# Kernel optimization log

Measured on AMD Instinct MI355X. Metric: run time of the kernel, lower is better.

## Reference

```python
import jax, jax.numpy as jnp
import numpy as np

T = 4096
MOL = 2048
DESC = 6
NSOL = 5
H = 2048
D_BLOCK = MOL + DESC            # 2054
FUSE = D_BLOCK * (1 + NSOL)     # 12324
D_IN = FUSE + 1                 # 12325
BOUNDARY_RF = 0.5
CLAMP_LO, CLAMP_HI = 1e-4, 1.0 - 1e-4


def setup_inputs() -> dict:
    key = jax.random.key(0)
    ks = jax.random.split(key, 32)
    s = 0.02  # weight init scale for numerical stability
    d = {
        "mol_vec": jax.random.normal(ks[0], (MOL,), jnp.float32),
        "solvent_seq": jax.random.uniform(ks[1], (T, NSOL), jnp.float32),
        "desc_seq": jax.random.normal(ks[2], (T, DESC), jnp.float32),
        "rf_true": jax.random.uniform(ks[3], (T,), jnp.float32),
        "solvent_vecs": jax.random.normal(ks[4], (NSOL, MOL), jnp.float32),
    }
    wshapes = [
        ("Wf0", (H, D_IN)), ("Wf1", (H, H)), ("Wf2", (H, H)), ("Wof", (1, H)),
        ("Wb0", (H, D_IN)), ("Wb1", (H, H)), ("Wb2", (H, H)), ("Wob", (1, H)),
    ]
    for i, (name, shp) in enumerate(wshapes):
        d[name] = jax.random.normal(ks[5 + i], shp, jnp.float32) * s
    for name, shp in [("bf0", (H,)), ("bf1", (H,)), ("bf2", (H,)), ("bof", (1,)),
                      ("bb0", (H,)), ("bb1", (H,)), ("bb2", (H,)), ("bob", (1,))]:
        d[name] = jnp.zeros(shp, jnp.float32)
    return d


def _step_features(mol_vec, solvent_seq, desc_seq, solvent_vecs):
    # mol_vec [MOL]; solvent_seq [T,NSOL]; desc_seq [T,DESC]; solvent_vecs [NSOL,MOL]
    mol_cat = jnp.concatenate(
        [jnp.broadcast_to(mol_vec, (T, MOL)), desc_seq], axis=-1)  # [T, D_BLOCK]
    scaled = solvent_seq[:, :, None] * solvent_vecs[None, :, :]      # [T,NSOL,MOL]
    sol_block = jnp.concatenate(
        [scaled, jnp.broadcast_to(desc_seq[:, None, :], (T, NSOL, DESC))], axis=-1)
    sol_flat = sol_block.reshape(T, NSOL * D_BLOCK)
    return jnp.concatenate([mol_cat, sol_flat], axis=-1)             # [T, FUSE]


def _trunk(x, W0, b0, W1, b1, W2, b2):
    # 3 Linear+GELU blocks (dropout is identity in eval)
    h = jax.nn.gelu(x @ W0.T + b0, approximate=False)
    h = jax.nn.gelu(h @ W1.T + b1, approximate=False)
    h = jax.nn.gelu(h @ W2.T + b2, approximate=False)
    return h


def reference(mol_vec, solvent_seq, desc_seq, rf_true, solvent_vecs,
              Wf0, bf0, Wf1, bf1, Wf2, bf2, Wof, bof,
              Wb0, bb0, Wb1, bb1, Wb2, bb2, Wob, bob):
    x = _step_features(mol_vec, solvent_seq, desc_seq, solvent_vecs)  # [T, FUSE]
    rf = jax.lax.stop_gradient(rf_true)  # teacher signal is detached
    b = jnp.asarray([BOUNDARY_RF], dtype=x.dtype)
    prev = jnp.concatenate([b, rf[:-1]])  # fwd branch sees rf_true[t-1]
    nxt = jnp.concatenate([rf[1:], b])    # bwd branch sees rf_true[t+1]

    inp_f = jnp.concatenate([x, prev[:, None]], axis=-1)  # [T, D_IN]
    inp_b = jnp.concatenate([x, nxt[:, None]], axis=-1)

    hf = _trunk(inp_f, Wf0, bf0, Wf1, bf1, Wf2, bf2)
    hb = _trunk(inp_b, Wb0, bb0, Wb1, bb1, Wb2, bb2)
    rf_fwd = (hf @ Wof.T + bof).squeeze(-1)  # [T]
    rf_bwd = (hb @ Wob.T + bob).squeeze(-1)
    rf_fwd = jnp.clip(rf_fwd, CLAMP_LO, CLAMP_HI)
    rf_bwd = jnp.clip(rf_bwd, CLAMP_LO, CLAMP_HI)
    return rf_fwd, rf_bwd
```

## Files before the change

kernel.cpp:

```cpp
#include <hip/hip_runtime.h>
#include <hip/hip_fp16.h>
#include <math.h>

#define T_DIM 4096
#define MOL_N 2048
#define DESC_N 6
#define NSOL_N 5
#define H_DIM 2048
#define DBLK 2054
#define D_IN_N 12325

typedef _Float16 f16x8 __attribute__((ext_vector_type(8)));
typedef float f32x4 __attribute__((ext_vector_type(4)));

__device__ __forceinline__ float gelu_f(float x) {
    float v = x * (1.5957691f + 0.0713548f * x * x);
    float e = __expf(-v);
    return x / (1.0f + e);
}

__global__ __launch_bounds__(256) void fold_kernel(
    const float* __restrict__ W0f, const float* __restrict__ W0b,
    const float* __restrict__ b0f, const float* __restrict__ b0b,
    const float* __restrict__ mol, const float* __restrict__ sv,
    float* __restrict__ fold_f, float* __restrict__ fold_b)
{
    const int h = blockIdx.x;
    const int z = blockIdx.y;
    const float* __restrict__ W0 = z ? W0b : W0f;
    const float* __restrict__ b0 = z ? b0b : b0f;
    float* __restrict__ fold = z ? fold_b : fold_f;
    const float* __restrict__ row = W0 + (size_t)h * D_IN_N;
    const int tid = threadIdx.x;

    float acc[6] = {0.f, 0.f, 0.f, 0.f, 0.f, 0.f};
    #pragma unroll
    for (int i = 0; i < 8; ++i) {
        const int c = tid + i * 256;
        const float m = mol[c];
        acc[0] += row[c] * m;
        #pragma unroll
        for (int s = 0; s < NSOL_N; ++s)
            acc[1 + s] += row[DBLK * (s + 1) + c] * sv[s * MOL_N + c];
    }
    #pragma unroll
    for (int i = 0; i < 6; ++i) {
        float v = acc[i];
        #pragma unroll
        for (int off = 32; off >= 1; off >>= 1)
            v += __shfl_xor(v, off, 64);
        acc[i] = v;
    }
    __shared__ float red[4][6];
    const int lane = tid & 63, wave = tid >> 6;
    if (lane == 0) {
        #pragma unroll
        for (int i = 0; i < 6; ++i) red[wave][i] = acc[i];
    }
    __syncthreads();
    if (tid < 6) {
        float s = red[0][tid] + red[1][tid] + red[2][tid] + red[3][tid];
        if (tid == 0) fold[h] = s + b0[h];
        else fold[(size_t)tid * H_DIM + h] = s;
    }
    if (tid >= 64 && tid < 70) {
        int j = tid - 64;
        float w = row[MOL_N + j];
        #pragma unroll
        for (int s = 0; s < NSOL_N; ++s) w += row[DBLK * (s + 1) + MOL_N + j];
        fold[(size_t)(6 + j) * H_DIM + h] = w;
    }
    if (tid == 70) fold[(size_t)12 * H_DIM + h] = row[D_IN_N - 1];
}

__global__ __launch_bounds__(256) void conv_kernel(
    const float* __restrict__ W1f, const float* __restrict__ W2f,
    const float* __restrict__ W1b, const float* __restrict__ W2b,
    _Float16* __restrict__ dstbase)
{
    const int z = blockIdx.y;
    const float* __restrict__ src = (z == 0) ? W1f : (z == 1) ? W2f : (z == 2) ? W1b : W2b;
    _Float16* __restrict__ dst = dstbase + (size_t)z * H_DIM * H_DIM;
    const int idx = blockIdx.x * 256 + threadIdx.x;
    float4 v = ((const float4*)src)[idx];
    struct h4 { _Float16 a, b, c, d; };
    h4 o;
    o.a = (_Float16)v.x; o.b = (_Float16)v.y; o.c = (_Float16)v.z; o.d = (_Float16)v.w;
    ((h4*)dst)[idx] = o;
}

__global__ __launch_bounds__(256) void h0_kernel(
    const float* __restrict__ fold_f, const float* __restrict__ fold_b,
    const float* __restrict__ desc, const float* __restrict__ sol,
    const float* __restrict__ rf,
    _Float16* __restrict__ h0f, _Float16* __restrict__ h0b)
{
    const int z = blockIdx.z;
    const float* __restrict__ fold = z ? fold_b : fold_f;
    _Float16* __restrict__ h0 = z ? h0b : h0f;
    const int h = blockIdx.x * 256 + threadIdx.x;
    const int tbase = blockIdx.y * 64;

    const float c0 = fold[h];
    float u[NSOL_N], wd[DESC_N];
    #pragma unroll
    for (int s = 0; s < NSOL_N; ++s) u[s] = fold[(size_t)(1 + s) * H_DIM + h];
    #pragma unroll
    for (int j = 0; j < DESC_N; ++j) wd[j] = fold[(size_t)(6 + j) * H_DIM + h];
    const float wp = fold[(size_t)12 * H_DIM + h];

    for (int i = 0; i < 64; ++i) {
        const int t = tbase + i;
        float pv;
        if (z == 0) pv = (t == 0) ? 0.5f : rf[t - 1];
        else        pv = (t == T_DIM - 1) ? 0.5f : rf[t + 1];
        float pre = c0 + wp * pv;
        #pragma unroll
        for (int s = 0; s < NSOL_N; ++s) pre += u[s] * sol[t * NSOL_N + s];
        #pragma unroll
        for (int j = 0; j < DESC_N; ++j) pre += wd[j] * desc[t * DESC_N + j];
        h0[(size_t)t * H_DIM + h] = (_Float16)gelu_f(pre);
    }
}

__global__ __launch_bounds__(256) void gemm_kernel(
    const _Float16* __restrict__ Af, const _Float16* __restrict__ Ab,
    const _Float16* __restrict__ Wfp, const _Float16* __restrict__ Wbp,
    const float* __restrict__ bfp, const float* __restrict__ bbp,
    _Float16* __restrict__ Cf, _Float16* __restrict__ Cb)
{
    constexpr int K = H_DIM;
    constexpr int N = H_DIM;
    const int bid = blockIdx.x;
    const int xcd = bid & 7;
    const int slot = bid >> 3;
    const int z = xcd & 1;
    const int q = xcd >> 1;
    const int m0 = (q * 8 + (slot & 7)) * 128;
    const int n0 = (slot >> 3) * 128;

    const _Float16* __restrict__ A = z ? Ab : Af;
    const _Float16* __restrict__ W = z ? Wbp : Wfp;
    const float* __restrict__ bias = z ? bbp : bfp;
    _Float16* __restrict__ C = z ? Cb : Cf;

    __shared__ _Float16 sA[128 * 64];
    __shared__ _Float16 sB[128 * 64];

    const int tid = threadIdx.x;
    const int wave = tid >> 6;
    const int lane = tid & 63;
    const int quad = lane >> 4;

    char* sAc = (char*)sA;
    char* sBc = (char*)sB;

    const _Float16* gA[4];
    const _Float16* gB[4];
    #pragma unroll
    for (int ld = 0; ld < 4; ++ld) {
        const int j = ld * 256 + tid;
        const int r = j >> 3;
        const int c = (j & 7) ^ (r & 7);
        gA[ld] = A + (size_t)(m0 + r) * K + c * 8;
        gB[ld] = W + (size_t)(n0 + r) * K + c * 8;
    }

    f32x4 acc[4][4];
    #pragma unroll
    for (int i = 0; i < 4; ++i)
        #pragma unroll
        for (int j = 0; j < 4; ++j)
            acc[i][j] = (f32x4){0.f, 0.f, 0.f, 0.f};

    const int rA = (wave & 1) * 64 + (lane & 15);
    const int rB = (wave >> 1) * 64 + (lane & 15);
    const int xorL = lane & 7;

    for (int k0 = 0; k0 < K; k0 += 64) {
        #pragma unroll
        for (int ld = 0; ld < 4; ++ld)
            __builtin_amdgcn_global_load_lds(
                (const __attribute__((address_space(1))) void*)(gA[ld] + k0),
                (__attribute__((address_space(3))) void*)(sAc + ld * 4096 + wave * 1024), 16, 0, 0);
        #pragma unroll
        for (int ld = 0; ld < 4; ++ld)
            __builtin_amdgcn_global_load_lds(
                (const __attribute__((address_space(1))) void*)(gB[ld] + k0),
                (__attribute__((address_space(3))) void*)(sBc + ld * 4096 + wave * 1024), 16, 0, 0);
        __syncthreads();
        #pragma unroll
        for (int kk = 0; kk < 2; ++kk) {
            const int coff = ((kk * 4 + quad) ^ xorL) * 16;
            f16x8 aF[4], bF[4];
            #pragma unroll
            for (int mi = 0; mi < 4; ++mi)
                aF[mi] = *(const f16x8*)(sAc + (rA + mi * 16) * 128 + coff);
            #pragma unroll
            for (int ni = 0; ni < 4; ++ni)
                bF[ni] = *(const f16x8*)(sBc + (rB + ni * 16) * 128 + coff);
            #pragma unroll
            for (int mi = 0; mi < 4; ++mi)
                #pragma unroll
                for (int ni = 0; ni < 4; ++ni)
                    acc[mi][ni] = __builtin_amdgcn_mfma_f32_16x16x32_f16(aF[mi], bF[ni], acc[mi][ni], 0, 0, 0);
        }
        __syncthreads();
    }

    const int colC = lane & 15;
    #pragma unroll
    for (int ni = 0; ni < 4; ++ni) {
        const int n = n0 + (wave >> 1) * 64 + ni * 16 + colC;
        const float bv = bias[n];
        #pragma unroll
        for (int mi = 0; mi < 4; ++mi) {
            const int mb = m0 + (wave & 1) * 64 + mi * 16 + quad * 4;
            #pragma unroll
            for (int r = 0; r < 4; ++r) {
                float v = acc[mi][ni][r] + bv;
                C[(size_t)(mb + r) * N + n] = (_Float16)gelu_f(v);
            }
        }
    }
}

__global__ __launch_bounds__(256) void gemm_out_kernel(
    const _Float16* __restrict__ Af, const _Float16* __restrict__ Ab,
    const _Float16* __restrict__ Wfp, const _Float16* __restrict__ Wbp,
    const float* __restrict__ bfp, const float* __restrict__ bbp,
    const float* __restrict__ Wof, const float* __restrict__ Wob,
    float* __restrict__ out_acc)
{
    constexpr int K = H_DIM;
    const int bid = blockIdx.x;
    const int xcd = bid & 7;
    const int slot = bid >> 3;
    const int z = xcd & 1;
    const int q = xcd >> 1;
    const int m0 = (q * 8 + (slot & 7)) * 128;
    const int n0 = (slot >> 3) * 128;

    const _Float16* __restrict__ A = z ? Ab : Af;
    const _Float16* __restrict__ W = z ? Wbp : Wfp;
    const float* __restrict__ bias = z ? bbp : bfp;
    const float* __restrict__ Wo = z ? Wob : Wof;

    __shared__ _Float16 sA[128 * 64];
    __shared__ _Float16 sB[128 * 64];

    const int tid = threadIdx.x;
    const int wave = tid >> 6;
    const int lane = tid & 63;
    const int quad = lane >> 4;

    char* sAc = (char*)sA;
    char* sBc = (char*)sB;

    const _Float16* gA[4];
    const _Float16* gB[4];
    #pragma unroll
    for (int ld = 0; ld < 4; ++ld) {
        const int j = ld * 256 + tid;
        const int r = j >> 3;
        const int c = (j & 7) ^ (r & 7);
        gA[ld] = A + (size_t)(m0 + r) * K + c * 8;
        gB[ld] = W + (size_t)(n0 + r) * K + c * 8;
    }

    f32x4 acc[4][4];
    #pragma unroll
    for (int i = 0; i < 4; ++i)
        #pragma unroll
        for (int j = 0; j < 4; ++j)
            acc[i][j] = (f32x4){0.f, 0.f, 0.f, 0.f};

    const int rA = (wave & 1) * 64 + (lane & 15);
    const int rB = (wave >> 1) * 64 + (lane & 15);
    const int xorL = lane & 7;

    for (int k0 = 0; k0 < K; k0 += 64) {
        #pragma unroll
        for (int ld = 0; ld < 4; ++ld)
            __builtin_amdgcn_global_load_lds(
                (const __attribute__((address_space(1))) void*)(gA[ld] + k0),
                (__attribute__((address_space(3))) void*)(sAc + ld * 4096 + wave * 1024), 16, 0, 0);
        #pragma unroll
        for (int ld = 0; ld < 4; ++ld)
            __builtin_amdgcn_global_load_lds(
                (const __attribute__((address_space(1))) void*)(gB[ld] + k0),
                (__attribute__((address_space(3))) void*)(sBc + ld * 4096 + wave * 1024), 16, 0, 0);
        __syncthreads();
        #pragma unroll
        for (int kk = 0; kk < 2; ++kk) {
            const int coff = ((kk * 4 + quad) ^ xorL) * 16;
            f16x8 aF[4], bF[4];
            #pragma unroll
            for (int mi = 0; mi < 4; ++mi)
                aF[mi] = *(const f16x8*)(sAc + (rA + mi * 16) * 128 + coff);
            #pragma unroll
            for (int ni = 0; ni < 4; ++ni)
                bF[ni] = *(const f16x8*)(sBc + (rB + ni * 16) * 128 + coff);
            #pragma unroll
            for (int mi = 0; mi < 4; ++mi)
                #pragma unroll
                for (int ni = 0; ni < 4; ++ni)
                    acc[mi][ni] = __builtin_amdgcn_mfma_f32_16x16x32_f16(aF[mi], bF[ni], acc[mi][ni], 0, 0, 0);
        }
        __syncthreads();
    }

    const int colC = lane & 15;
    float bv[4], wo[4];
    #pragma unroll
    for (int ni = 0; ni < 4; ++ni) {
        const int n = n0 + (wave >> 1) * 64 + ni * 16 + colC;
        bv[ni] = bias[n];
        wo[ni] = Wo[n];
    }
    #pragma unroll
    for (int mi = 0; mi < 4; ++mi) {
        #pragma unroll
        for (int r = 0; r < 4; ++r) {
            float s = 0.f;
            #pragma unroll
            for (int ni = 0; ni < 4; ++ni)
                s += gelu_f(acc[mi][ni][r] + bv[ni]) * wo[ni];
            s += __shfl_xor(s, 1, 64);
            s += __shfl_xor(s, 2, 64);
            s += __shfl_xor(s, 4, 64);
            s += __shfl_xor(s, 8, 64);
            if (colC == 0) {
                const int row = m0 + (wave & 1) * 64 + mi * 16 + quad * 4 + r;
                atomicAdd(&out_acc[z * T_DIM + row], s);
            }
        }
    }
}

__global__ __launch_bounds__(256) void finalize_kernel(
    const float* __restrict__ out_acc,
    const float* __restrict__ bof, const float* __restrict__ bob,
    float* __restrict__ out)
{
    const int idx = blockIdx.x * 256 + threadIdx.x;
    const int z = idx >> 12;
    float v = out_acc[idx] + (z ? bob[0] : bof[0]);
    v = fminf(fmaxf(v, 1e-4f), 1.0f - 1e-4f);
    out[idx] = v;
}

extern "C" void kernel_launch(void* const* d_in, const int* in_sizes, int n_in,
                              void* d_out, int out_size, void* d_ws, size_t ws_size,
                              hipStream_t stream)
{
    (void)in_sizes; (void)n_in; (void)out_size; (void)ws_size;
    const float* mol = (const float*)d_in[0];
    const float* sol = (const float*)d_in[1];
    const float* desc = (const float*)d_in[2];
    const float* rf  = (const float*)d_in[3];
    const float* sv  = (const float*)d_in[4];
    const float* Wf0 = (const float*)d_in[5];
    const float* Wf1 = (const float*)d_in[6];
    const float* Wf2 = (const float*)d_in[7];
    const float* Wof = (const float*)d_in[8];
    const float* Wb0 = (const float*)d_in[9];
    const float* Wb1 = (const float*)d_in[10];
    const float* Wb2 = (const float*)d_in[11];
    const float* Wob = (const float*)d_in[12];
    const float* bf0 = (const float*)d_in[13];
    const float* bf1 = (const float*)d_in[14];
    const float* bf2 = (const float*)d_in[15];
    const float* bof = (const float*)d_in[16];
    const float* bb0 = (const float*)d_in[17];
    const float* bb1 = (const float*)d_in[18];
    const float* bb2 = (const float*)d_in[19];
    const float* bob = (const float*)d_in[20];
    float* out = (float*)d_out;

    char* ws = (char*)d_ws;
    float* fold_f = (float*)(ws + 0);
    float* fold_b = (float*)(ws + 131072);
    _Float16* Wc = (_Float16*)(ws + 262144);
    const size_t WSZ = (size_t)H_DIM * H_DIM;
    _Float16* W1f_c = Wc;
    _Float16* W2f_c = Wc + WSZ;
    _Float16* W1b_c = Wc + 2 * WSZ;
    _Float16* W2b_c = Wc + 3 * WSZ;
    const size_t HSZ = (size_t)T_DIM * H_DIM;
    _Float16* h0f = (_Float16*)(ws + 33816576);
    _Float16* h0b = h0f + HSZ;
    _Float16* h1f = (_Float16*)(ws + 33816576 + 2 * 16777216);
    _Float16* h1b = h1f + HSZ;
    float* out_acc = (float*)(ws + 33816576);

    fold_kernel<<<dim3(H_DIM, 2), 256, 0, stream>>>(Wf0, Wb0, bf0, bb0, mol, sv, fold_f, fold_b);
    conv_kernel<<<dim3(H_DIM * H_DIM / 1024, 4), 256, 0, stream>>>(Wf1, Wf2, Wb1, Wb2, Wc);
    h0_kernel<<<dim3(8, 64, 2), 256, 0, stream>>>(fold_f, fold_b, desc, sol, rf, h0f, h0b);
    gemm_kernel<<<dim3(1024), 256, 0, stream>>>(h0f, h0b, W1f_c, W1b_c, bf1, bb1, h1f, h1b);
    hipMemsetAsync(out_acc, 0, 2 * T_DIM * sizeof(float), stream);
    gemm_out_kernel<<<dim3(1024), 256, 0, stream>>>(h1f, h1b, W2f_c, W2b_c, bf2, bb2, Wof, Wob, out_acc);
    finalize_kernel<<<dim3(2 * T_DIM / 256), 256, 0, stream>>>(out_acc, bof, bob, out);
}
```

Baseline: 493.0 us.

## Use 256x256 tiled GEMMs with 4-stage LDS pipeline and merge prep kernels

Replaces the 128x128 single-buffered GEMM with a shared 256x256-tile core that uses 512 threads, BK=32, and a four-buffer global_load_lds pipeline. Waits are done with explicit vmcnt counts and raw barriers, and MFMA priority is raised. The weight-conversion and fold kernels are merged into one launch. The output GEMM now writes per-N-tile partials via an LDS reduction instead of atomics, which removes the memset, and finalize sums the eight partials. Only 256 blocks now cover 256 CUs, so per-CU load balance and the 128KB LDS footprint matter.

```diff
diff --git a/kernel.cpp b/kernel.cpp
--- a/kernel.cpp
+++ b/kernel.cpp
@@ -9,6 +9,7 @@
 #define H_DIM 2048
 #define DBLK 2054
 #define D_IN_N 12325
+#define GK 2048
 
 typedef _Float16 f16x8 __attribute__((ext_vector_type(8)));
 typedef float f32x4 __attribute__((ext_vector_type(4)));
@@ -19,19 +20,39 @@
     return x / (1.0f + e);
 }
 
-__global__ __launch_bounds__(256) void fold_kernel(
+__global__ __launch_bounds__(256) void prep_kernel(
+    const float* __restrict__ W1f, const float* __restrict__ W2f,
+    const float* __restrict__ W1b, const float* __restrict__ W2b,
+    _Float16* __restrict__ Wc,
     const float* __restrict__ W0f, const float* __restrict__ W0b,
     const float* __restrict__ b0f, const float* __restrict__ b0b,
     const float* __restrict__ mol, const float* __restrict__ sv,
     float* __restrict__ fold_f, float* __restrict__ fold_b)
 {
-    const int h = blockIdx.x;
-    const int z = blockIdx.y;
+    __shared__ float red[4][6];
+    const int bid = blockIdx.x;
+    const int tid = threadIdx.x;
+
+    if (bid < 16384) {
+        const int z = bid >> 12;
+        const float* __restrict__ src = (z == 0) ? W1f : (z == 1) ? W2f : (z == 2) ? W1b : W2b;
+        _Float16* __restrict__ dst = Wc + (size_t)z * H_DIM * H_DIM;
+        const int idx = (bid & 4095) * 256 + tid;
+        float4 v = ((const float4*)src)[idx];
+        struct h4 { _Float16 a, b, c, d; };
+        h4 o;
+        o.a = (_Float16)v.x; o.b = (_Float16)v.y; o.c = (_Float16)v.z; o.d = (_Float16)v.w;
+        ((h4*)dst)[idx] = o;
+        return;
+    }
+
+    const int fb = bid - 16384;
+    const int h = fb & 2047;
+    const int z = fb >> 11;
     const float* __restrict__ W0 = z ? W0b : W0f;
     const float* __restrict__ b0 = z ? b0b : b0f;
     float* __restrict__ fold = z ? fold_b : fold_f;
     const float* __restrict__ row = W0 + (size_t)h * D_IN_N;
-    const int tid = threadIdx.x;
 
     float acc[6] = {0.f, 0.f, 0.f, 0.f, 0.f, 0.f};
     #pragma unroll
@@ -51,7 +72,6 @@
             v += __shfl_xor(v, off, 64);
         acc[i] = v;
     }
-    __shared__ float red[4][6];
     const int lane = tid & 63, wave = tid >> 6;
     if (lane == 0) {
         #pragma unroll
@@ -71,22 +91,6 @@
         fold[(size_t)(6 + j) * H_DIM + h] = w;
     }
     if (tid == 70) fold[(size_t)12 * H_DIM + h] = row[D_IN_N - 1];
-}
-
-__global__ __launch_bounds__(256) void conv_kernel(
-    const float* __restrict__ W1f, const float* __restrict__ W2f,
-    const float* __restrict__ W1b, const float* __restrict__ W2b,
-    _Float16* __restrict__ dstbase)
-{
-    const int z = blockIdx.y;
-    const float* __restrict__ src = (z == 0) ? W1f : (z == 1) ? W2f : (z == 2) ? W1b : W2b;
-    _Float16* __restrict__ dst = dstbase + (size_t)z * H_DIM * H_DIM;
-    const int idx = blockIdx.x * 256 + threadIdx.x;
-    float4 v = ((const float4*)src)[idx];
-    struct h4 { _Float16 a, b, c, d; };
-    h4 o;
-    o.a = (_Float16)v.x; o.b = (_Float16)v.y; o.c = (_Float16)v.z; o.d = (_Float16)v.w;
-    ((h4*)dst)[idx] = o;
 }
 
 __global__ __launch_bounds__(256) void h0_kernel(
@@ -123,203 +127,182 @@
     }
 }
 
-__global__ __launch_bounds__(256) void gemm_kernel(
+__device__ __forceinline__ void gemm_core256(
+    const _Float16* __restrict__ A, const _Float16* __restrict__ W,
+    const int m0, const int n0, char* sc, f32x4 (&acc)[8][4])
+{
+    const int tid = threadIdx.x;
+    const int wave = tid >> 6;
+    const int lane = tid & 63;
+    const int t15 = lane & 15;
+    const int quad = lane >> 4;
+    const int wr = wave >> 2;
+    const int wc = wave & 3;
+    const int poff = (quad ^ ((t15 >> 1) & 3)) * 16;
+    const int aoff0 = (wr * 128 + t15) * 64 + poff;
+    const int boff0 = 16384 + (wc * 64 + t15) * 64 + poff;
+
+    const _Float16* gsrc[4];
+    #pragma unroll
+    for (int ld = 0; ld < 4; ++ld) {
+        const int j = (ld & 1) * 512 + tid;
+        const int r = j >> 2;
+        const int c = (j & 3) ^ ((r >> 1) & 3);
+        gsrc[ld] = ((ld < 2) ? (A + (size_t)(m0 + r) * GK)
+                             : (W + (size_t)(n0 + r) * GK)) + c * 8;
+    }
+
+    #pragma unroll
+    for (int mi = 0; mi < 8; ++mi)
+        #pragma unroll
+        for (int ni = 0; ni < 4; ++ni)
+            acc[mi][ni] = (f32x4){0.f, 0.f, 0.f, 0.f};
+
+#define STAGE_T(kt, b) do { \
+    char* _db = sc + (b) * 32768; \
+    const int _ko = (kt) * 32; \
+    __builtin_amdgcn_global_load_lds((const __attribute__((address_space(1))) void*)(gsrc[0] + _ko), (__attribute__((address_space(3))) void*)(_db + wave * 1024), 16, 0, 0); \
+    __builtin_amdgcn_global_load_lds((const __attribute__((address_space(1))) void*)(gsrc[1] + _ko), (__attribute__((address_space(3))) void*)(_db + 8192 + wave * 1024), 16, 0, 0); \
+    __builtin_amdgcn_global_load_lds((const __attribute__((address_space(1))) void*)(gsrc[2] + _ko), (__attribute__((address_space(3))) void*)(_db + 16384 + wave * 1024), 16, 0, 0); \
+    __builtin_amdgcn_global_load_lds((const __attribute__((address_space(1))) void*)(gsrc[3] + _ko), (__attribute__((address_space(3))) void*)(_db + 24576 + wave * 1024), 16, 0, 0); \
+} while (0)
+
+#define COMPUTE_T(b) do { \
+    const char* _db = sc + (b) * 32768; \
+    f16x8 aF[8], bF[4]; \
+    _Pragma("unroll") \
+    for (int mi = 0; mi < 8; ++mi) aF[mi] = *(const f16x8*)(_db + aoff0 + mi * 1024); \
+    _Pragma("unroll") \
+    for (int ni = 0; ni < 4; ++ni) bF[ni] = *(const f16x8*)(_db + boff0 + ni * 1024); \
+    __builtin_amdgcn_s_setprio(1); \
+    _Pragma("unroll") \
+    for (int mi = 0; mi < 8; ++mi) { \
+        _Pragma("unroll") \
+        for (int ni = 0; ni < 4; ++ni) \
+            acc[mi][ni] = __builtin_amdgcn_mfma_f32_16x16x32_f16(aF[mi], bF[ni], acc[mi][ni], 0, 0, 0); \
+    } \
+    __builtin_amdgcn_s_setprio(0); \
+    asm volatile("s_waitcnt lgkmcnt(0)" ::: "memory"); \
+} while (0)
+
+    STAGE_T(0, 0); STAGE_T(1, 1); STAGE_T(2, 2);
+
+    #pragma unroll 1
+    for (int k4 = 0; k4 < 60; k4 += 4) {
+        asm volatile("s_waitcnt vmcnt(8)" ::: "memory");
+        __builtin_amdgcn_s_barrier();
+        STAGE_T(k4 + 3, 3); COMPUTE_T(0);
+        asm volatile("s_waitcnt vmcnt(8)" ::: "memory");
+        __builtin_amdgcn_s_barrier();
+        STAGE_T(k4 + 4, 0); COMPUTE_T(1);
+        asm volatile("s_waitcnt vmcnt(8)" ::: "memory");
+        __builtin_amdgcn_s_barrier();
+        STAGE_T(k4 + 5, 1); COMPUTE_T(2);
+        asm volatile("s_waitcnt vmcnt(8)" ::: "memory");
+        __builtin_amdgcn_s_barrier();
+        STAGE_T(k4 + 6, 2); COMPUTE_T(3);
+    }
+    asm volatile("s_waitcnt vmcnt(8)" ::: "memory");
+    __builtin_amdgcn_s_barrier();
+    STAGE_T(63, 3); COMPUTE_T(0);
+    asm volatile("s_waitcnt vmcnt(8)" ::: "memory");
+    __builtin_amdgcn_s_barrier();
+    COMPUTE_T(1);
+    asm volatile("s_waitcnt vmcnt(4)" ::: "memory");
+    __builtin_amdgcn_s_barrier();
+    COMPUTE_T(2);
+    asm volatile("s_waitcnt vmcnt(0)" ::: "memory");
+    __builtin_amdgcn_s_barrier();
+    COMPUTE_T(3);
+
+#undef STAGE_T
+#undef COMPUTE_T
+}
+
+__global__ __launch_bounds__(512, 2) void gemm1_kernel(
     const _Float16* __restrict__ Af, const _Float16* __restrict__ Ab,
     const _Float16* __restrict__ Wfp, const _Float16* __restrict__ Wbp,
     const float* __restrict__ bfp, const float* __restrict__ bbp,
     _Float16* __restrict__ Cf, _Float16* __restrict__ Cb)
 {
-    constexpr int K = H_DIM;
-    constexpr int N = H_DIM;
+    __shared__ _Float16 smem[65536];
+    char* sc = (char*)smem;
     const int bid = blockIdx.x;
     const int xcd = bid & 7;
     const int slot = bid >> 3;
     const int z = xcd & 1;
     const int q = xcd >> 1;
-    const int m0 = (q * 8 + (slot & 7)) * 128;
-    const int n0 = (slot >> 3) * 128;
+    const int m0 = (q * 4 + (slot & 3)) * 256;
+    const int n0 = (slot >> 2) * 256;
 
     const _Float16* __restrict__ A = z ? Ab : Af;
     const _Float16* __restrict__ W = z ? Wbp : Wfp;
     const float* __restrict__ bias = z ? bbp : bfp;
     _Float16* __restrict__ C = z ? Cb : Cf;
 
-    __shared__ _Float16 sA[128 * 64];
-    __shared__ _Float16 sB[128 * 64];
+    f32x4 acc[8][4];
+    gemm_core256(A, W, m0, n0, sc, acc);
 
     const int tid = threadIdx.x;
-    const int wave = tid >> 6;
-    const int lane = tid & 63;
-    const int quad = lane >> 4;
-
-    char* sAc = (char*)sA;
-    char* sBc = (char*)sB;
-
-    const _Float16* gA[4];
-    const _Float16* gB[4];
-    #pragma unroll
-    for (int ld = 0; ld < 4; ++ld) {
-        const int j = ld * 256 + tid;
-        const int r = j >> 3;
-        const int c = (j & 7) ^ (r & 7);
-        gA[ld] = A + (size_t)(m0 + r) * K + c * 8;
-        gB[ld] = W + (size_t)(n0 + r) * K + c * 8;
-    }
-
-    f32x4 acc[4][4];
-    #pragma unroll
-    for (int i = 0; i < 4; ++i)
-        #pragma unroll
-        for (int j = 0; j < 4; ++j)
-            acc[i][j] = (f32x4){0.f, 0.f, 0.f, 0.f};
-
-    const int rA = (wave & 1) * 64 + (lane & 15);
-    const int rB = (wave >> 1) * 64 + (lane & 15);
-    const int xorL = lane & 7;
-
-    for (int k0 = 0; k0 < K; k0 += 64) {
-        #pragma unroll
-        for (int ld = 0; ld < 4; ++ld)
-            __builtin_amdgcn_global_load_lds(
-                (const __attribute__((address_space(1))) void*)(gA[ld] + k0),
-                (__attribute__((address_space(3))) void*)(sAc + ld * 4096 + wave * 1024), 16, 0, 0);
-        #pragma unroll
-        for (int ld = 0; ld < 4; ++ld)
-            __builtin_amdgcn_global_load_lds(
-                (const __attribute__((address_space(1))) void*)(gB[ld] + k0),
-                (__attribute__((address_space(3))) void*)(sBc + ld * 4096 + wave * 1024), 16, 0, 0);
-        __syncthreads();
-        #pragma unroll
-        for (int kk = 0; kk < 2; ++kk) {
-            const int coff = ((kk * 4 + quad) ^ xorL) * 16;
-            f16x8 aF[4], bF[4];
+    const int wave = tid >> 6, lane = tid & 63;
+    const int colC = lane & 15, quad = lane >> 4;
+    const int wr = wave >> 2, wc = wave & 3;
+    #pragma unroll
+    for (int ni = 0; ni < 4; ++ni) {
+        const int n = n0 + wc * 64 + ni * 16 + colC;
+        const float bv = bias[n];
+        #pragma unroll
+        for (int mi = 0; mi < 8; ++mi) {
+            const int mb = m0 + wr * 128 + mi * 16 + quad * 4;
             #pragma unroll
-            for (int mi = 0; mi < 4; ++mi)
-                aF[mi] = *(const f16x8*)(sAc + (rA + mi * 16) * 128 + coff);
-            #pragma unroll
-            for (int ni = 0; ni < 4; ++ni)
-                bF[ni] = *(const f16x8*)(sBc + (rB + ni * 16) * 128 + coff);
-            #pragma unroll
-            for (int mi = 0; mi < 4; ++mi)
-                #pragma unroll
-                for (int ni = 0; ni < 4; ++ni)
-                    acc[mi][ni] = __builtin_amdgcn_mfma_f32_16x16x32_f16(aF[mi], bF[ni], acc[mi][ni], 0, 0, 0);
+            for (int r = 0; r < 4; ++r)
+                C[(size_t)(mb + r) * H_DIM + n] = (_Float16)gelu_f(acc[mi][ni][r] + bv);
         }
-        __syncthreads();
-    }
-
-    const int colC = lane & 15;
-    #pragma unroll
-    for (int ni = 0; ni < 4; ++ni) {
-        const int n = n0 + (wave >> 1) * 64 + ni * 16 + colC;
-        const float bv = bias[n];
-        #pragma unroll
-        for (int mi = 0; mi < 4; ++mi) {
-            const int mb = m0 + (wave & 1) * 64 + mi * 16 + quad * 4;
-            #pragma unroll
-            for (int r = 0; r < 4; ++r) {
-                float v = acc[mi][ni][r] + bv;
-                C[(size_t)(mb + r) * N + n] = (_Float16)gelu_f(v);
-            }
-        }
-    }
-}
-
-__global__ __launch_bounds__(256) void gemm_out_kernel(
+    }
+}
+
+__global__ __launch_bounds__(512, 2) void gemm_out_kernel(
     const _Float16* __restrict__ Af, const _Float16* __restrict__ Ab,
     const _Float16* __restrict__ Wfp, const _Float16* __restrict__ Wbp,
     const float* __restrict__ bfp, const float* __restrict__ bbp,
     const float* __restrict__ Wof, const float* __restrict__ Wob,
-    float* __restrict__ out_acc)
-{
-    constexpr int K = H_DIM;
+    float* __restrict__ partial)
+{
+    __shared__ _Float16 smem[65536];
+    char* sc = (char*)smem;
     const int bid = blockIdx.x;
     const int xcd = bid & 7;
     const int slot = bid >> 3;
     const int z = xcd & 1;
     const int q = xcd >> 1;
-    const int m0 = (q * 8 + (slot & 7)) * 128;
-    const int n0 = (slot >> 3) * 128;
+    const int m0 = (q * 4 + (slot & 3)) * 256;
+    const int n0 = (slot >> 2) * 256;
 
     const _Float16* __restrict__ A = z ? Ab : Af;
     const _Float16* __restrict__ W = z ? Wbp : Wfp;
     const float* __restrict__ bias = z ? bbp : bfp;
     const float* __restrict__ Wo = z ? Wob : Wof;
 
-    __shared__ _Float16 sA[128 * 64];
-    __shared__ _Float16 sB[128 * 64];
+    f32x4 acc[8][4];
+    gemm_core256(A, W, m0, n0, sc, acc);
 
     const int tid = threadIdx.x;
-    const int wave = tid >> 6;
-    const int lane = tid & 63;
-    const int quad = lane >> 4;
-
-    char* sAc = (char*)sA;
-    char* sBc = (char*)sB;
-
-    const _Float16* gA[4];
-    const _Float16* gB[4];
-    #pragma unroll
-    for (int ld = 0; ld < 4; ++ld) {
-        const int j = ld * 256 + tid;
-        const int r = j >> 3;
-        const int c = (j & 7) ^ (r & 7);
-        gA[ld] = A + (size_t)(m0 + r) * K + c * 8;
-        gB[ld] = W + (size_t)(n0 + r) * K + c * 8;
-    }
-
-    f32x4 acc[4][4];
-    #pragma unroll
-    for (int i = 0; i < 4; ++i)
-        #pragma unroll
-        for (int j = 0; j < 4; ++j)
-            acc[i][j] = (f32x4){0.f, 0.f, 0.f, 0.f};
-
-    const int rA = (wave & 1) * 64 + (lane & 15);
-    const int rB = (wave >> 1) * 64 + (lane & 15);
-    const int xorL = lane & 7;
-
-    for (int k0 = 0; k0 < K; k0 += 64) {
-        #pragma unroll
-        for (int ld = 0; ld < 4; ++ld)
-            __builtin_amdgcn_global_load_lds(
-                (const __attribute__((address_space(1))) void*)(gA[ld] + k0),
-                (__attribute__((address_space(3))) void*)(sAc + ld * 4096 + wave * 1024), 16, 0, 0);
-        #pragma unroll
-        for (int ld = 0; ld < 4; ++ld)
-            __builtin_amdgcn_global_load_lds(
-                (const __attribute__((address_space(1))) void*)(gB[ld] + k0),
-                (__attribute__((address_space(3))) void*)(sBc + ld * 4096 + wave * 1024), 16, 0, 0);
-        __syncthreads();
-        #pragma unroll
-        for (int kk = 0; kk < 2; ++kk) {
-            const int coff = ((kk * 4 + quad) ^ xorL) * 16;
-            f16x8 aF[4], bF[4];
-            #pragma unroll
-            for (int mi = 0; mi < 4; ++mi)
-                aF[mi] = *(const f16x8*)(sAc + (rA + mi * 16) * 128 + coff);
-            #pragma unroll
-            for (int ni = 0; ni < 4; ++ni)
-                bF[ni] = *(const f16x8*)(sBc + (rB + ni * 16) * 128 + coff);
-            #pragma unroll
-            for (int mi = 0; mi < 4; ++mi)
-                #pragma unroll
-                for (int ni = 0; ni < 4; ++ni)
-                    acc[mi][ni] = __builtin_amdgcn_mfma_f32_16x16x32_f16(aF[mi], bF[ni], acc[mi][ni], 0, 0, 0);
-        }
-        __syncthreads();
-    }
-
-    const int colC = lane & 15;
+    const int wave = tid >> 6, lane = tid & 63;
+    const int colC = lane & 15, quad = lane >> 4;
+    const int wr = wave >> 2, wc = wave & 3;
+
     float bv[4], wo[4];
     #pragma unroll
     for (int ni = 0; ni < 4; ++ni) {
-        const int n = n0 + (wave >> 1) * 64 + ni * 16 + colC;
+        const int n = n0 + wc * 64 + ni * 16 + colC;
         bv[ni] = bias[n];
         wo[ni] = Wo[n];
     }
-    #pragma unroll
-    for (int mi = 0; mi < 4; ++mi) {
+
+    __syncthreads();
+    float* red = (float*)sc;
+    #pragma unroll
+    for (int mi = 0; mi < 8; ++mi) {
         #pragma unroll
         for (int r = 0; r < 4; ++r) {
             float s = 0.f;
@@ -330,22 +313,30 @@
             s += __shfl_xor(s, 2, 64);
             s += __shfl_xor(s, 4, 64);
             s += __shfl_xor(s, 8, 64);
-            if (colC == 0) {
-                const int row = m0 + (wave & 1) * 64 + mi * 16 + quad * 4 + r;
-                atomicAdd(&out_acc[z * T_DIM + row], s);
-            }
+            if (colC == 0)
+                red[wc * 256 + wr * 128 + mi * 16 + quad * 4 + r] = s;
         }
     }
+    __syncthreads();
+    if (tid < 256) {
+        float v = red[tid] + red[256 + tid] + red[512 + tid] + red[768 + tid];
+        const int n_tile = slot >> 2;
+        partial[((size_t)z * 8 + n_tile) * T_DIM + m0 + tid] = v;
+    }
 }
 
 __global__ __launch_bounds__(256) void finalize_kernel(
-    const float* __restrict__ out_acc,
+    const float* __restrict__ partial,
     const float* __restrict__ bof, const float* __restrict__ bob,
     float* __restrict__ out)
 {
     const int idx = blockIdx.x * 256 + threadIdx.x;
     const int z = idx >> 12;
-    float v = out_acc[idx] + (z ? bob[0] : bof[0]);
+    const int row = idx & 4095;
+    float v = z ? bob[0] : bof[0];
+    #pragma unroll
+    for (int nt = 0; nt < 8; ++nt)
+        v += partial[((size_t)z * 8 + nt) * T_DIM + row];
     v = fminf(fmaxf(v, 1e-4f), 1.0f - 1e-4f);
     out[idx] = v;
 }
@@ -392,13 +383,12 @@
     _Float16* h0b = h0f + HSZ;
     _Float16* h1f = (_Float16*)(ws + 33816576 + 2 * 16777216);
     _Float16* h1b = h1f + HSZ;
-    float* out_acc = (float*)(ws + 33816576);
-
-    fold_kernel<<<dim3(H_DIM, 2), 256, 0, stream>>>(Wf0, Wb0, bf0, bb0, mol, sv, fold_f, fold_b);
-    conv_kernel<<<dim3(H_DIM * H_DIM / 1024, 4), 256, 0, stream>>>(Wf1, Wf2, Wb1, Wb2, Wc);
+    float* partial = (float*)(ws + 33816576);
+
+    prep_kernel<<<dim3(20480), 256, 0, stream>>>(
+        Wf1, Wf2, Wb1, Wb2, Wc, Wf0, Wb0, bf0, bb0, mol, sv, fold_f, fold_b);
     h0_kernel<<<dim3(8, 64, 2), 256, 0, stream>>>(fold_f, fold_b, desc, sol, rf, h0f, h0b);
-    gemm_kernel<<<dim3(1024), 256, 0, stream>>>(h0f, h0b, W1f_c, W1b_c, bf1, bb1, h1f, h1b);
-    hipMemsetAsync(out_acc, 0, 2 * T_DIM * sizeof(float), stream);
-    gemm_out_kernel<<<dim3(1024), 256, 0, stream>>>(h1f, h1b, W2f_c, W2b_c, bf2, bb2, Wof, Wob, out_acc);
-    finalize_kernel<<<dim3(2 * T_DIM / 256), 256, 0, stream>>>(out_acc, bof, bob, out);
-}
+    gemm1_kernel<<<dim3(256), 512, 0, stream>>>(h0f, h0b, W1f_c, W1b_c, bf1, bb1, h1f, h1b);
+    gemm_out_kernel<<<dim3(256), 512, 0, stream>>>(h1f, h1b, W2f_c, W2b_c, bf2, bb2, Wof, Wob, partial);
+    finalize_kernel<<<dim3(32), 256, 0, stream>>>(partial, bof, bob, out);
+}
```

Result: faster. 465.8 us (-5.5%).
